# Kernel optimization log

Measured on AMD Instinct MI355X. Metric: run time of the kernel, lower is better.

## Reference

```python
import jax, jax.numpy as jnp
import numpy as np

INPUT_SIZE = 2
HIDDEN_SIZE = 5
OUTPUT_SIZE = 1
SEQ_LEN = 512
BATCH = 8192


def setup_inputs() -> dict:
    key = jax.random.key(0)
    ks = jax.random.split(key, 7)
    H, I = HIDDEN_SIZE, INPUT_SIZE
    bound = 1.0 / np.sqrt(H)  # PyTorch nn.LSTM / nn.Linear init range
    x = jax.random.normal(ks[0], (SEQ_LEN, BATCH, I), dtype=jnp.float32)
    W_ih = jax.random.uniform(ks[1], (4 * H, I), minval=-bound, maxval=bound, dtype=jnp.float32)
    W_hh = jax.random.uniform(ks[2], (4 * H, H), minval=-bound, maxval=bound, dtype=jnp.float32)
    b_ih = jax.random.uniform(ks[3], (4 * H,), minval=-bound, maxval=bound, dtype=jnp.float32)
    b_hh = jax.random.uniform(ks[4], (4 * H,), minval=-bound, maxval=bound, dtype=jnp.float32)
    W_lin = jax.random.uniform(ks[5], (OUTPUT_SIZE, H), minval=-bound, maxval=bound, dtype=jnp.float32)
    b_lin = jax.random.uniform(ks[6], (OUTPUT_SIZE,), minval=-bound, maxval=bound, dtype=jnp.float32)
    return {"x": x, "W_ih": W_ih, "W_hh": W_hh, "b_ih": b_ih, "b_hh": b_hh,
            "W_lin": W_lin, "b_lin": b_lin}


def _lstm_last_hidden(x, W_ih, W_hh, b_ih, b_hh):
    # x: [S, B, I]. Precompute the input projection as one big GEMM,
    # then scan the recurrence. PyTorch gate order: i, f, g, o.
    S, B, _ = x.shape
    H = W_hh.shape[1]
    x_proj = jnp.einsum('sbi,gi->sbg', x, W_ih) + b_ih + b_hh  # [S, B, 4H]

    def step(carry, xp):
        h, c = carry
        gates = xp + h @ W_hh.T  # [B, 4H]
        i, f, g, o = jnp.split(gates, 4, axis=-1)
        i = jax.nn.sigmoid(i)
        f = jax.nn.sigmoid(f)
        g = jnp.tanh(g)
        o = jax.nn.sigmoid(o)
        c = f * c + i * g
        h = o * jnp.tanh(c)
        return (h, c), None

    h0 = jnp.zeros((B, H), dtype=x.dtype)
    c0 = jnp.zeros((B, H), dtype=x.dtype)
    (h_last, _), _ = jax.lax.scan(step, (h0, c0), x_proj)
    return h_last  # [B, H]


def reference(x, W_ih, W_hh, b_ih, b_hh, W_lin, b_lin):
    # Original applies the linear to all timesteps then takes the last row;
    # mathematically identical (and cheaper) to project only the last hidden state.
    h_last = _lstm_last_hidden(x, W_ih, W_hh, b_ih, b_hh)
    return h_last @ W_lin.T + b_lin  # [B, OUTPUT_SIZE]
```

## Files before the change

kernel.cpp:

```cpp
#include <hip/hip_runtime.h>

constexpr int S = 512, B = 8192, H = 5;
constexpr float KN1 = -1.44269504088896340736f;
constexpr float KN2 = 2.0f * KN1;

__device__ __forceinline__ float fexp2(float x) { return __builtin_amdgcn_exp2f(x); }
__device__ __forceinline__ float frcp(float x)  { return __builtin_amdgcn_rcpf(x); }

#define SWZ(v, imm) __int_as_float(__builtin_amdgcn_ds_swizzle(__float_as_int(v), (imm)))

__global__ __launch_bounds__(256, 1) void lstm_kernel(
    const float* __restrict__ x,
    const float* __restrict__ W_ih,
    const float* __restrict__ W_hh,
    const float* __restrict__ b_ih,
    const float* __restrict__ b_hh,
    const float* __restrict__ W_lin,
    const float* __restrict__ b_lin,
    float* __restrict__ out)
{
  const int tid   = blockIdx.x * blockDim.x + threadIdx.x;
  const int chain = tid >> 3;
  const int j     = tid & 7;
  const int jm    = (j < H) ? j : H - 1;

  float wi0[4], wi1[4], wh[4][H], bb[4];
  #pragma unroll
  for (int t = 0; t < 4; ++t) {
    const int g = t * H + jm;
    const float s = (t == 2) ? KN2 : KN1;
    wi0[t] = W_ih[g * 2 + 0] * s;
    wi1[t] = W_ih[g * 2 + 1] * s;
    #pragma unroll
    for (int k = 0; k < H; ++k) wh[t][k] = W_hh[g * H + k] * s;
    bb[t] = (b_ih[g] + b_hh[g]) * s;
  }

  float h = 0.0f, c = 0.0f;
  float hg[H] = {0, 0, 0, 0, 0};

  const float2* __restrict__ x2 = (const float2*)x;

  auto step = [&](float2 xv) {
    float a[4];
    #pragma unroll
    for (int t = 0; t < 4; ++t) {
      float v = fmaf(xv.x, wi0[t], bb[t]);
      v = fmaf(xv.y, wi1[t], v);
      #pragma unroll
      for (int k = 0; k < H; ++k) v = fmaf(hg[k], wh[t][k], v);
      a[t] = v;
    }
    const float iv = frcp(1.0f + fexp2(a[0]));
    const float fv = frcp(1.0f + fexp2(a[1]));
    const float gv = fmaf(2.0f, frcp(1.0f + fexp2(a[2])), -1.0f);
    const float ov = frcp(1.0f + fexp2(a[3]));
    c = fmaf(fv, c, iv * gv);
    const float th = fmaf(2.0f, frcp(1.0f + fexp2(c * KN2)), -1.0f);
    h = ov * th;
    hg[0] = SWZ(h, 0x018);
    hg[1] = SWZ(h, 0x038);
    hg[2] = SWZ(h, 0x058);
    hg[3] = SWZ(h, 0x078);
    hg[4] = SWZ(h, 0x098);
  };

  constexpr int CH = 4;
  float2 buf0[CH], buf1[CH];
  #pragma unroll
  for (int u = 0; u < CH; ++u) buf0[u] = x2[(size_t)u * B + chain];

  for (int t0 = 0; t0 < S; t0 += 2 * CH) {
    #pragma unroll
    for (int u = 0; u < CH; ++u) buf1[u] = x2[(size_t)(t0 + CH + u) * B + chain];
    #pragma unroll
    for (int u = 0; u < CH; ++u) step(buf0[u]);
    if (t0 + 2 * CH < S) {
      #pragma unroll
      for (int u = 0; u < CH; ++u) buf0[u] = x2[(size_t)(t0 + 2 * CH + u) * B + chain];
    }
    #pragma unroll
    for (int u = 0; u < CH; ++u) step(buf1[u]);
  }

  float p = (j < H) ? h * W_lin[jm] : 0.0f;
  p += SWZ(p, 0x41F);
  p += SWZ(p, 0x81F);
  p += SWZ(p, 0x101F);
  if (j == 0) out[chain] = p + b_lin[0];
}

extern "C" void kernel_launch(void* const* d_in, const int* in_sizes, int n_in,
                              void* d_out, int out_size, void* d_ws, size_t ws_size,
                              hipStream_t stream) {
  const float* x     = (const float*)d_in[0];
  const float* W_ih  = (const float*)d_in[1];
  const float* W_hh  = (const float*)d_in[2];
  const float* b_ih  = (const float*)d_in[3];
  const float* b_hh  = (const float*)d_in[4];
  const float* W_lin = (const float*)d_in[5];
  const float* b_lin = (const float*)d_in[6];
  float* out = (float*)d_out;

  const int threads = B * 8;
  dim3 grid(threads / 256), block(256);
  hipLaunchKernelGGL(lstm_kernel, grid, block, 0, stream,
                     x, W_ih, W_hh, b_ih, b_hh, W_lin, b_lin, out);
}
```

Before: 85.06 us.

## Split LSTM gates across 16 lanes per chain, exchanging i*g via DPP

Each batch chain now uses 16 lanes instead of 8. One half of the lanes computes the input and candidate gates, the other half computes the forget and output gates, so each lane does only two gate dot products and two transcendentals per step. The i*g product is passed to the other half with a DPP row rotate, and the hidden state is broadcast from the upper half with ds_swizzle. This shortens the serial per-step dependency chain, at the cost of twice as many threads and waves, redundant cell-state work in the lower half, and an extra cross-lane hop each step.

```diff
diff --git a/kernel.cpp b/kernel.cpp
--- a/kernel.cpp
+++ b/kernel.cpp
@@ -8,8 +8,9 @@
 __device__ __forceinline__ float frcp(float x)  { return __builtin_amdgcn_rcpf(x); }
 
 #define SWZ(v, imm) __int_as_float(__builtin_amdgcn_ds_swizzle(__float_as_int(v), (imm)))
+#define ROR8(v) __int_as_float(__builtin_amdgcn_mov_dpp(__float_as_int(v), 0x128, 0xF, 0xF, false))
 
-__global__ __launch_bounds__(256, 1) void lstm_kernel(
+__global__ __launch_bounds__(256, 2) void lstm_kernel(
     const float* __restrict__ x,
     const float* __restrict__ W_ih,
     const float* __restrict__ W_hh,
@@ -20,21 +21,28 @@
     float* __restrict__ out)
 {
   const int tid   = blockIdx.x * blockDim.x + threadIdx.x;
-  const int chain = tid >> 3;
-  const int j     = tid & 7;
+  const int chain = tid >> 4;
+  const int l     = tid & 15;
+  const int u     = l >> 3;
+  const int j     = l & 7;
   const int jm    = (j < H) ? j : H - 1;
 
-  float wi0[4], wi1[4], wh[4][H], bb[4];
+  const int r1 = (u ? H : 0) + jm;
+  const int r2 = (u ? 3 * H : 2 * H) + jm;
+  const float s2 = u ? KN1 : KN2;
+  const float eA = u ? 1.0f : 2.0f;
+  const float eB = u ? 0.0f : -1.0f;
+
+  float w1x0 = W_ih[r1 * 2 + 0] * KN1, w1x1 = W_ih[r1 * 2 + 1] * KN1;
+  float w2x0 = W_ih[r2 * 2 + 0] * s2,  w2x1 = W_ih[r2 * 2 + 1] * s2;
+  float w1h[H], w2h[H];
   #pragma unroll
-  for (int t = 0; t < 4; ++t) {
-    const int g = t * H + jm;
-    const float s = (t == 2) ? KN2 : KN1;
-    wi0[t] = W_ih[g * 2 + 0] * s;
-    wi1[t] = W_ih[g * 2 + 1] * s;
-    #pragma unroll
-    for (int k = 0; k < H; ++k) wh[t][k] = W_hh[g * H + k] * s;
-    bb[t] = (b_ih[g] + b_hh[g]) * s;
+  for (int k = 0; k < H; ++k) {
+    w1h[k] = W_hh[r1 * H + k] * KN1;
+    w2h[k] = W_hh[r2 * H + k] * s2;
   }
+  const float b1 = (b_ih[r1] + b_hh[r1]) * KN1;
+  const float b2 = (b_ih[r2] + b_hh[r2]) * s2;
 
   float h = 0.0f, c = 0.0f;
   float hg[H] = {0, 0, 0, 0, 0};
@@ -42,52 +50,53 @@
   const float2* __restrict__ x2 = (const float2*)x;
 
   auto step = [&](float2 xv) {
-    float a[4];
+    float a1 = fmaf(xv.x, w1x0, b1);
+    a1 = fmaf(xv.y, w1x1, a1);
+    float a2 = fmaf(xv.x, w2x0, b2);
+    a2 = fmaf(xv.y, w2x1, a2);
     #pragma unroll
-    for (int t = 0; t < 4; ++t) {
-      float v = fmaf(xv.x, wi0[t], bb[t]);
-      v = fmaf(xv.y, wi1[t], v);
-      #pragma unroll
-      for (int k = 0; k < H; ++k) v = fmaf(hg[k], wh[t][k], v);
-      a[t] = v;
+    for (int k = 0; k < H; ++k) {
+      a1 = fmaf(hg[k], w1h[k], a1);
+      a2 = fmaf(hg[k], w2h[k], a2);
     }
-    const float iv = frcp(1.0f + fexp2(a[0]));
-    const float fv = frcp(1.0f + fexp2(a[1]));
-    const float gv = fmaf(2.0f, frcp(1.0f + fexp2(a[2])), -1.0f);
-    const float ov = frcp(1.0f + fexp2(a[3]));
-    c = fmaf(fv, c, iv * gv);
+    const float v1 = frcp(1.0f + fexp2(a1));
+    const float r2v = frcp(1.0f + fexp2(a2));
+    const float go = fmaf(r2v, eA, eB);
+    const float p  = v1 * go;
+    const float pr = ROR8(p);
+    c = fmaf(v1, c, pr);
     const float th = fmaf(2.0f, frcp(1.0f + fexp2(c * KN2)), -1.0f);
-    h = ov * th;
-    hg[0] = SWZ(h, 0x018);
-    hg[1] = SWZ(h, 0x038);
-    hg[2] = SWZ(h, 0x058);
-    hg[3] = SWZ(h, 0x078);
-    hg[4] = SWZ(h, 0x098);
+    h = go * th;
+    hg[0] = SWZ(h, 0x110);
+    hg[1] = SWZ(h, 0x130);
+    hg[2] = SWZ(h, 0x150);
+    hg[3] = SWZ(h, 0x170);
+    hg[4] = SWZ(h, 0x190);
   };
 
   constexpr int CH = 4;
   float2 buf0[CH], buf1[CH];
   #pragma unroll
-  for (int u = 0; u < CH; ++u) buf0[u] = x2[(size_t)u * B + chain];
+  for (int t = 0; t < CH; ++t) buf0[t] = x2[(size_t)t * B + chain];
 
   for (int t0 = 0; t0 < S; t0 += 2 * CH) {
     #pragma unroll
-    for (int u = 0; u < CH; ++u) buf1[u] = x2[(size_t)(t0 + CH + u) * B + chain];
+    for (int t = 0; t < CH; ++t) buf1[t] = x2[(size_t)(t0 + CH + t) * B + chain];
     #pragma unroll
-    for (int u = 0; u < CH; ++u) step(buf0[u]);
+    for (int t = 0; t < CH; ++t) step(buf0[t]);
     if (t0 + 2 * CH < S) {
       #pragma unroll
-      for (int u = 0; u < CH; ++u) buf0[u] = x2[(size_t)(t0 + 2 * CH + u) * B + chain];
+      for (int t = 0; t < CH; ++t) buf0[t] = x2[(size_t)(t0 + 2 * CH + t) * B + chain];
     }
     #pragma unroll
-    for (int u = 0; u < CH; ++u) step(buf1[u]);
+    for (int t = 0; t < CH; ++t) step(buf1[t]);
   }
 
-  float p = (j < H) ? h * W_lin[jm] : 0.0f;
+  float p = (u == 1 && j < H) ? h * W_lin[jm] : 0.0f;
   p += SWZ(p, 0x41F);
   p += SWZ(p, 0x81F);
   p += SWZ(p, 0x101F);
-  if (j == 0) out[chain] = p + b_lin[0];
+  if ((tid & 15) == 8) out[chain] = p + b_lin[0];
 }
 
 extern "C" void kernel_launch(void* const* d_in, const int* in_sizes, int n_in,
@@ -102,7 +111,7 @@
   const float* b_lin = (const float*)d_in[6];
   float* out = (float*)d_out;
 
-  const int threads = B * 8;
+  const int threads = B * 16;
   dim3 grid(threads / 256), block(256);
   hipLaunchKernelGGL(lstm_kernel, grid, block, 0, stream,
                      x, W_ih, W_hh, b_ih, b_hh, W_lin, b_lin, out);
```

After: 81.54 us. 1.04x faster.

## Spread LSTM gates across 32 lanes per chain with one gate row per lane

Applied to the files above, without the earlier changes.

Each batch chain now uses 32 lanes instead of 8, with each lane computing a single gate row rather than all four gates of one hidden unit. Gate activations are combined across lanes using ds_swizzle and a DPP row rotate to build the cell update, and the h broadcast and final reduction are rewritten to match. The aim is to shorten the serial per-step dependency chain by spreading the gate work across more lanes. In exchange it launches four times as many threads, leaves several lanes idle, and adds extra cross-lane latency to every step.

```diff
diff --git a/kernel.cpp b/kernel.cpp
--- a/kernel.cpp
+++ b/kernel.cpp
@@ -8,8 +8,9 @@
 __device__ __forceinline__ float frcp(float x)  { return __builtin_amdgcn_rcpf(x); }
 
 #define SWZ(v, imm) __int_as_float(__builtin_amdgcn_ds_swizzle(__float_as_int(v), (imm)))
+#define ROR5(v) __int_as_float(__builtin_amdgcn_mov_dpp(__float_as_int(v), 0x125, 0xF, 0xF, false))
 
-__global__ __launch_bounds__(256, 1) void lstm_kernel(
+__global__ __launch_bounds__(256, 4) void lstm_kernel(
     const float* __restrict__ x,
     const float* __restrict__ W_ih,
     const float* __restrict__ W_hh,
@@ -20,49 +21,54 @@
     float* __restrict__ out)
 {
   const int tid   = blockIdx.x * blockDim.x + threadIdx.x;
-  const int chain = tid >> 3;
-  const int j     = tid & 7;
-  const int jm    = (j < H) ? j : H - 1;
+  const int chain = tid >> 5;
+  const int q     = tid & 31;
 
-  float wi0[4], wi1[4], wh[4][H], bb[4];
+  int t, j;
+  if      (q < 5)  { t = 0; j = q; }
+  else if (q < 10) { t = 1; j = q - 5; }
+  else if (q < 16) { t = 0; j = 0; }
+  else if (q < 21) { t = 2; j = q - 16; }
+  else if (q < 26) { t = 3; j = q - 21; }
+  else             { t = 0; j = 0; }
+  const int   r  = t * H + j;
+  const float s  = (t == 2) ? KN2 : KN1;
+  const float eA = (t == 2) ? 2.0f * KN2 : 1.0f;
+  const float eB = (t == 2) ? -KN2 : 0.0f;
+
+  const float wx0 = W_ih[r * 2 + 0] * s;
+  const float wx1 = W_ih[r * 2 + 1] * s;
+  float wh[H];
   #pragma unroll
-  for (int t = 0; t < 4; ++t) {
-    const int g = t * H + jm;
-    const float s = (t == 2) ? KN2 : KN1;
-    wi0[t] = W_ih[g * 2 + 0] * s;
-    wi1[t] = W_ih[g * 2 + 1] * s;
-    #pragma unroll
-    for (int k = 0; k < H; ++k) wh[t][k] = W_hh[g * H + k] * s;
-    bb[t] = (b_ih[g] + b_hh[g]) * s;
-  }
+  for (int k = 0; k < H; ++k) wh[k] = W_hh[r * H + k] * s;
+  const float bb = (b_ih[r] + b_hh[r]) * s;
 
-  float h = 0.0f, c = 0.0f;
+  float CS = 0.0f, h = 0.0f;
   float hg[H] = {0, 0, 0, 0, 0};
 
   const float2* __restrict__ x2 = (const float2*)x;
 
   auto step = [&](float2 xv) {
-    float a[4];
+    float a = fmaf(xv.x, wx0, bb);
+    a = fmaf(xv.y, wx1, a);
     #pragma unroll
-    for (int t = 0; t < 4; ++t) {
-      float v = fmaf(xv.x, wi0[t], bb[t]);
-      v = fmaf(xv.y, wi1[t], v);
-      #pragma unroll
-      for (int k = 0; k < H; ++k) v = fmaf(hg[k], wh[t][k], v);
-      a[t] = v;
-    }
-    const float iv = frcp(1.0f + fexp2(a[0]));
-    const float fv = frcp(1.0f + fexp2(a[1]));
-    const float gv = fmaf(2.0f, frcp(1.0f + fexp2(a[2])), -1.0f);
-    const float ov = frcp(1.0f + fexp2(a[3]));
-    c = fmaf(fv, c, iv * gv);
-    const float th = fmaf(2.0f, frcp(1.0f + fexp2(c * KN2)), -1.0f);
-    h = ov * th;
-    hg[0] = SWZ(h, 0x018);
-    hg[1] = SWZ(h, 0x038);
-    hg[2] = SWZ(h, 0x058);
-    hg[3] = SWZ(h, 0x078);
-    hg[4] = SWZ(h, 0x098);
+    for (int k = 0; k < H; ++k) a = fmaf(hg[k], wh[k], a);
+    const float e   = fexp2(a);
+    const float rv  = frcp(1.0f + e);
+    const float act = fmaf(rv, eA, eB);
+    const float asw = SWZ(act, 0x401F);
+    const float p   = act * asw;
+    const float pr  = ROR5(p);
+    CS = fmaf(act, CS, pr);
+    const float et = fexp2(CS);
+    const float rt = frcp(1.0f + et);
+    const float o2 = asw + asw;
+    h = fmaf(rt, o2, -asw);
+    hg[0] = SWZ(h, 0x0A0);
+    hg[1] = SWZ(h, 0x0C0);
+    hg[2] = SWZ(h, 0x0E0);
+    hg[3] = SWZ(h, 0x100);
+    hg[4] = SWZ(h, 0x120);
   };
 
   constexpr int CH = 4;
@@ -83,11 +89,13 @@
     for (int u = 0; u < CH; ++u) step(buf1[u]);
   }
 
-  float p = (j < H) ? h * W_lin[jm] : 0.0f;
-  p += SWZ(p, 0x41F);
-  p += SWZ(p, 0x81F);
-  p += SWZ(p, 0x101F);
-  if (j == 0) out[chain] = p + b_lin[0];
+  float pv = (q >= 5 && q < 10) ? h * W_lin[q - 5] : 0.0f;
+  pv += SWZ(pv, 0x041F);
+  pv += SWZ(pv, 0x081F);
+  pv += SWZ(pv, 0x101F);
+  pv += SWZ(pv, 0x201F);
+  pv += SWZ(pv, 0x401F);
+  if (q == 0) out[chain] = pv + b_lin[0];
 }
 
 extern "C" void kernel_launch(void* const* d_in, const int* in_sizes, int n_in,
@@ -102,7 +110,7 @@
   const float* b_lin = (const float*)d_in[6];
   float* out = (float*)d_out;
 
-  const int threads = B * 8;
+  const int threads = B * 32;
   dim3 grid(threads / 256), block(256);
   hipLaunchKernelGGL(lstm_kernel, grid, block, 0, stream,
                      x, W_ih, W_hh, b_ih, b_hh, W_lin, b_lin, out);
```

New measurement: 106.4 us. 25.0% more time.

## Pack gate FMAs into v2f packed math and replace swizzle broadcasts with DPP

Applied to the files above, without the earlier changes.

Gate pre-activations are now computed as two float2 vectors so the compiler can emit packed FP32 FMAs (v_pk_fma_f32), halving the FMA instruction count per step. The hidden-state broadcast within each 8-lane group moves from ds_swizzle (which goes through the LDS crossbar with higher latency) to DPP quad_perm and row moves with a select. The cell-state and tanh math is also folded to absorb scale constants, removing a few dependent ops on the serial recurrence path. The DPP path needs more instructions (two moves plus a select per element), and its correctness depends on the exact lane mapping.

```diff
diff --git a/kernel.cpp b/kernel.cpp
--- a/kernel.cpp
+++ b/kernel.cpp
@@ -1,4 +1,6 @@
 #include <hip/hip_runtime.h>
+
+typedef float v2f __attribute__((ext_vector_type(2)));
 
 constexpr int S = 512, B = 8192, H = 5;
 constexpr float KN1 = -1.44269504088896340736f;
@@ -8,6 +10,7 @@
 __device__ __forceinline__ float frcp(float x)  { return __builtin_amdgcn_rcpf(x); }
 
 #define SWZ(v, imm) __int_as_float(__builtin_amdgcn_ds_swizzle(__float_as_int(v), (imm)))
+#define DPP(v, ctrl) __int_as_float(__builtin_amdgcn_mov_dpp(__float_as_int(v), (ctrl), 0xF, 0xF, false))
 
 __global__ __launch_bounds__(256, 1) void lstm_kernel(
     const float* __restrict__ x,
@@ -24,70 +27,81 @@
   const int j     = tid & 7;
   const int jm    = (j < H) ? j : H - 1;
 
-  float wi0[4], wi1[4], wh[4][H], bb[4];
+  const int ri = jm, rf = H + jm, rg = 2 * H + jm, ro = 3 * H + jm;
+
+  const v2f wx0_1 = {W_ih[ri * 2 + 0] * KN1, W_ih[rf * 2 + 0] * KN1};
+  const v2f wx1_1 = {W_ih[ri * 2 + 1] * KN1, W_ih[rf * 2 + 1] * KN1};
+  const v2f wx0_2 = {W_ih[rg * 2 + 0] * KN2, W_ih[ro * 2 + 0] * KN1};
+  const v2f wx1_2 = {W_ih[rg * 2 + 1] * KN2, W_ih[ro * 2 + 1] * KN1};
+  v2f wh1[H], wh2[H];
   #pragma unroll
-  for (int t = 0; t < 4; ++t) {
-    const int g = t * H + jm;
-    const float s = (t == 2) ? KN2 : KN1;
-    wi0[t] = W_ih[g * 2 + 0] * s;
-    wi1[t] = W_ih[g * 2 + 1] * s;
-    #pragma unroll
-    for (int k = 0; k < H; ++k) wh[t][k] = W_hh[g * H + k] * s;
-    bb[t] = (b_ih[g] + b_hh[g]) * s;
+  for (int k = 0; k < H; ++k) {
+    wh1[k] = (v2f){W_hh[ri * H + k] * KN1, W_hh[rf * H + k] * KN1};
+    wh2[k] = (v2f){W_hh[rg * H + k] * KN2, W_hh[ro * H + k] * KN1};
   }
+  const v2f bb1 = {(b_ih[ri] + b_hh[ri]) * KN1, (b_ih[rf] + b_hh[rf]) * KN1};
+  const v2f bb2 = {(b_ih[rg] + b_hh[rg]) * KN2, (b_ih[ro] + b_hh[ro]) * KN1};
 
-  float h = 0.0f, c = 0.0f;
+  float CS = 0.0f, h = 0.0f;
   float hg[H] = {0, 0, 0, 0, 0};
 
   const float2* __restrict__ x2 = (const float2*)x;
 
   auto step = [&](float2 xv) {
-    float a[4];
+    v2f a1 = bb1, a2 = bb2;
+    a1 = __builtin_elementwise_fma((v2f){xv.x, xv.x}, wx0_1, a1);
+    a2 = __builtin_elementwise_fma((v2f){xv.x, xv.x}, wx0_2, a2);
+    a1 = __builtin_elementwise_fma((v2f){xv.y, xv.y}, wx1_1, a1);
+    a2 = __builtin_elementwise_fma((v2f){xv.y, xv.y}, wx1_2, a2);
     #pragma unroll
-    for (int t = 0; t < 4; ++t) {
-      float v = fmaf(xv.x, wi0[t], bb[t]);
-      v = fmaf(xv.y, wi1[t], v);
-      #pragma unroll
-      for (int k = 0; k < H; ++k) v = fmaf(hg[k], wh[t][k], v);
-      a[t] = v;
+    for (int k = 0; k < H; ++k) {
+      a1 = __builtin_elementwise_fma((v2f){hg[k], hg[k]}, wh1[k], a1);
+      a2 = __builtin_elementwise_fma((v2f){hg[k], hg[k]}, wh2[k], a2);
     }
-    const float iv = frcp(1.0f + fexp2(a[0]));
-    const float fv = frcp(1.0f + fexp2(a[1]));
-    const float gv = fmaf(2.0f, frcp(1.0f + fexp2(a[2])), -1.0f);
-    const float ov = frcp(1.0f + fexp2(a[3]));
-    c = fmaf(fv, c, iv * gv);
-    const float th = fmaf(2.0f, frcp(1.0f + fexp2(c * KN2)), -1.0f);
-    h = ov * th;
-    hg[0] = SWZ(h, 0x018);
-    hg[1] = SWZ(h, 0x038);
-    hg[2] = SWZ(h, 0x058);
-    hg[3] = SWZ(h, 0x078);
-    hg[4] = SWZ(h, 0x098);
+    const float si  = frcp(1.0f + fexp2(a1.x));
+    const float sf  = frcp(1.0f + fexp2(a1.y));
+    const float rgv = frcp(1.0f + fexp2(a2.x));
+    const float so  = frcp(1.0f + fexp2(a2.y));
+    const float gK  = fmaf(rgv, 2.0f * KN2, -KN2);
+    CS = fmaf(sf, CS, si * gK);
+    const float rt = frcp(1.0f + fexp2(CS));
+    h = fmaf(rt, so + so, -so);
+    const bool hi = (j & 4) != 0;
+    const float hm = DPP(h, 0x141);
+    hg[4] = hi ? h : hm;
+    const float s0 = DPP(h, 0x00), m0 = DPP(s0, 0x141);
+    hg[0] = hi ? m0 : s0;
+    const float s1 = DPP(h, 0x55), m1 = DPP(s1, 0x141);
+    hg[1] = hi ? m1 : s1;
+    const float s2 = DPP(h, 0xAA), m2 = DPP(s2, 0x141);
+    hg[2] = hi ? m2 : s2;
+    const float s3 = DPP(h, 0xFF), m3 = DPP(s3, 0x141);
+    hg[3] = hi ? m3 : s3;
   };
 
   constexpr int CH = 4;
   float2 buf0[CH], buf1[CH];
   #pragma unroll
-  for (int u = 0; u < CH; ++u) buf0[u] = x2[(size_t)u * B + chain];
+  for (int t = 0; t < CH; ++t) buf0[t] = x2[(size_t)t * B + chain];
 
   for (int t0 = 0; t0 < S; t0 += 2 * CH) {
     #pragma unroll
-    for (int u = 0; u < CH; ++u) buf1[u] = x2[(size_t)(t0 + CH + u) * B + chain];
+    for (int t = 0; t < CH; ++t) buf1[t] = x2[(size_t)(t0 + CH + t) * B + chain];
     #pragma unroll
-    for (int u = 0; u < CH; ++u) step(buf0[u]);
+    for (int t = 0; t < CH; ++t) step(buf0[t]);
     if (t0 + 2 * CH < S) {
       #pragma unroll
-      for (int u = 0; u < CH; ++u) buf0[u] = x2[(size_t)(t0 + 2 * CH + u) * B + chain];
+      for (int t = 0; t < CH; ++t) buf0[t] = x2[(size_t)(t0 + 2 * CH + t) * B + chain];
     }
     #pragma unroll
-    for (int u = 0; u < CH; ++u) step(buf1[u]);
+    for (int t = 0; t < CH; ++t) step(buf1[t]);
   }
 
-  float p = (j < H) ? h * W_lin[jm] : 0.0f;
-  p += SWZ(p, 0x41F);
-  p += SWZ(p, 0x81F);
-  p += SWZ(p, 0x101F);
-  if (j == 0) out[chain] = p + b_lin[0];
+  float pv = (j < H) ? h * W_lin[jm] : 0.0f;
+  pv += SWZ(pv, 0x041F);
+  pv += SWZ(pv, 0x081F);
+  pv += SWZ(pv, 0x101F);
+  if (j == 0) out[chain] = pv + b_lin[0];
 }
 
 extern "C" void kernel_launch(void* const* d_in, const int* in_sizes, int n_in,
```

Result: faster. 74.26 us (-12.7%).
